# Optimization experiments

Measured on AMD Instinct MI355X. Metric: run time of the kernel, lower is better.

Reference implementation:

```python
import jax, jax.numpy as jnp
import numpy as np

IN_SHAPE = 4096
H_S = 250        # sender_hidden
H_R = 100        # receiver_hidden
MAX_LEN = 30     # message_shape[0]
VOCAB = 40       # message_shape[1]; EOS = VOCAB-1
OUT_CLS = 512 ** 2  # out_shape[1] ** out_shape[0]


def lstm_cell(x, h, c, W_ih, W_hh, b_ih, b_hh):
    # PyTorch LSTM cell: gate order i, f, g, o
    gates = W_ih @ x + b_ih + W_hh @ h + b_hh
    i, f, g, o = jnp.split(gates, 4)
    c_new = jax.nn.sigmoid(f) * c + jax.nn.sigmoid(i) * jnp.tanh(g)
    h_new = jax.nn.sigmoid(o) * jnp.tanh(c_new)
    return h_new, c_new


def setup_inputs() -> dict:
    key = jax.random.key(0)
    ks = jax.random.split(key, 16)
    s = 0.05
    return {
        "x": jax.random.normal(ks[0], (IN_SHAPE,), dtype=jnp.float32),
        "gumbel_noise": jax.random.gumbel(ks[1], (MAX_LEN, VOCAB), dtype=jnp.float32),
        "W_s1": jax.random.normal(ks[2], (H_S, IN_SHAPE)) * s,
        "b_s1": jnp.zeros((H_S,), jnp.float32),
        "W_ih1": jax.random.normal(ks[3], (4 * H_S, VOCAB)) * s,
        "W_hh1": jax.random.normal(ks[4], (4 * H_S, H_S)) * s,
        "b_ih1": jnp.zeros((4 * H_S,), jnp.float32),
        "b_hh1": jnp.zeros((4 * H_S,), jnp.float32),
        "W_p": jax.random.normal(ks[5], (VOCAB, H_S)) * s,
        "b_p": jnp.zeros((VOCAB,), jnp.float32),
        "W_ih2": jax.random.normal(ks[6], (4 * H_R, VOCAB)) * s,
        "W_hh2": jax.random.normal(ks[7], (4 * H_R, H_R)) * s,
        "b_ih2": jnp.zeros((4 * H_R,), jnp.float32),
        "b_hh2": jnp.zeros((4 * H_R,), jnp.float32),
        "W_r": jax.random.normal(ks[8], (OUT_CLS, H_R)) * s,
        "b_r": jnp.zeros((OUT_CLS,), jnp.float32),
    }


def reference(x, gumbel_noise, W_s1, b_s1, W_ih1, W_hh1, b_ih1, b_hh1,
              W_p, b_p, W_ih2, W_hh2, b_ih2, b_hh2, W_r, b_r):
    dt = x.dtype
    eos = jax.nn.one_hot(VOCAB - 1, VOCAB, dtype=dt)
    # sender: h0 = relu(sender1(x)), c0 = 0, first input = sos = zeros
    h0 = jax.nn.relu(W_s1 @ x + b_s1)
    c0 = jnp.zeros((H_S,), dt)
    sos = jnp.zeros((VOCAB,), dt)
    is_last = jnp.arange(MAX_LEN) == MAX_LEN - 1

    def sender_step(carry, inp):
        h, c, sym, done = carry
        g, last = inp
        nh, nc = lstm_cell(sym, h, c, W_ih1, W_hh1, b_ih1, b_hh1)
        logits = W_p @ nh + b_p
        soft = jax.nn.softmax(logits + g)  # gumbel_softmax, tau=1
        idx = jnp.argmax(soft)
        hard = jax.nn.one_hot(idx, VOCAB, dtype=dt)
        st = hard + soft - jax.lax.stop_gradient(soft)  # straight-through
        # at max length the original appends the plain EOS constant
        emit = jnp.where(last & ~done, eos, st)
        emit = jnp.where(done, eos, emit)
        valid = ~done  # this symbol is part of the message
        new_done = done | (idx == VOCAB - 1) | last
        h = jnp.where(done, h, nh)
        c = jnp.where(done, c, nc)
        sym = jnp.where(done, sym, emit)
        return (h, c, sym, new_done), (emit, valid)

    _, (msg, valid) = jax.lax.scan(
        sender_step, (h0, c0, sos, jnp.array(False)), (gumbel_noise, is_last))

    # receiver LSTM: consume message up to and including first EOS (freeze after)
    def recv_step(carry, inp):
        h, c = carry
        sym, v = inp
        nh, nc = lstm_cell(sym, h, c, W_ih2, W_hh2, b_ih2, b_hh2)
        return (jnp.where(v, nh, h), jnp.where(v, nc, c)), None

    (hR, _), _ = jax.lax.scan(
        recv_step, (jnp.zeros((H_R,), dt), jnp.zeros((H_R,), dt)), (msg, valid))
    return jax.nn.softmax(W_r @ hR + b_r)  # [OUT_CLS]
```

## Files before the change

kernel.cpp:

```cpp
#include <hip/hip_runtime.h>
#include <math.h>

#define HS    250
#define HRr   100
#define VOC   40
#define TMAX  30
#define NCLS  262144
#define KS    10
#define RPB   25

#define WS_FLAGS 0
#define WS_MFLAG 32
#define WS_SUMS  64
#define WS_NH    448
#define WS_LP    960
#define WS_MSG   1792
#define WS_HR    3008

#define ATOMIC_ST_REL(p, v) __hip_atomic_store((p), (v), __ATOMIC_RELEASE, __HIP_MEMORY_SCOPE_AGENT)
#define ATOMIC_ST_RLX(p, v) __hip_atomic_store((p), (v), __ATOMIC_RELAXED, __HIP_MEMORY_SCOPE_AGENT)
#define ATOMIC_LD_RLX(p)    __hip_atomic_load((p), __ATOMIC_RELAXED, __HIP_MEMORY_SCOPE_AGENT)

__device__ __forceinline__ float sigf(float x) { return 1.f / (1.f + expf(-x)); }

__device__ __forceinline__ float lanebc(float v, int l) {
  return __int_as_float(__builtin_amdgcn_readlane(__float_as_int(v), l));
}

#define SENDER_GATES(P, HV)                                   \
  {                                                           \
    _Pragma("unroll")                                         \
    for (int i = 0; i < 64; i += 4) {                         \
      a0 += whh[i    ] * lanebc(HV, i    );                   \
      a1 += whh[i + 1] * lanebc(HV, i + 1);                   \
      a2 += whh[i + 2] * lanebc(HV, i + 2);                   \
      a3 += whh[i + 3] * lanebc(HV, i + 3);                   \
    }                                                         \
    _Pragma("unroll")                                         \
    for (int i = 0; i < 10; i += 2) {                         \
      a0 += wih[i    ] * lanebc(sv, (P) * 10 + i    );        \
      a1 += wih[i + 1] * lanebc(sv, (P) * 10 + i + 1);        \
    }                                                         \
  }

#define RED(x) ((part[(x)] + part[100 + (x)]) + (part[200 + (x)] + part[300 + (x)]))

#define SPIN_FLAGS(need_)                                                     \
  {                                                                           \
    int v;                                                                    \
    do {                                                                      \
      v = (lane < KS) ? ATOMIC_LD_RLX(&flags[lane]) : (need_);                \
    } while (!__all(v >= (need_)));                                           \
  }

__global__ __launch_bounds__(512, 2) void k_sender(
    const float* __restrict__ x,
    const float* __restrict__ W_s1,  const float* __restrict__ b_s1,
    const float* __restrict__ gum,
    const float* __restrict__ W_ih1, const float* __restrict__ W_hh1,
    const float* __restrict__ b_ih1, const float* __restrict__ b_hh1,
    const float* __restrict__ W_p,   const float* __restrict__ b_p,
    const float* __restrict__ W_ih2, const float* __restrict__ W_hh2,
    const float* __restrict__ b_ih2, const float* __restrict__ b_hh2,
    float* __restrict__ ws) {
  __shared__ float part[512];
  __shared__ float symL[VOC];
  __shared__ float h0L[32];
  __shared__ int   ctrl;
  __shared__ float gL[400];
  __shared__ float hL[HRr];
  __shared__ int   rawL;

  const int b    = blockIdx.x;
  const int t0   = threadIdx.x;
  const int lane = t0 & 63;
  const int w    = t0 >> 6;

  int*   flags = (int*)ws;
  int*   mflag = (int*)ws + WS_MFLAG;
  float* nh    = ws + WS_NH;
  float* lp    = ws + WS_LP;
  float* msg   = ws + WS_MSG;

  if (b < KS) {
    const int p    = w & 3;
    const int lr   = ((w >> 2) << 6) + lane;
    const bool gact = (lr < 100);
    const int gi   = lr / 25, rr = lr % 25;
    const int grow = gi * 250 + b * RPB + rr;

    float whh[64], wih[10], bsum = 0.f;
    if (gact) {
      #pragma unroll
      for (int i = 0; i < 64; i++) {
        int k = p * 64 + i;
        whh[i] = (k < HS) ? W_hh1[(size_t)grow * HS + k] : 0.f;
      }
      #pragma unroll
      for (int i = 0; i < 10; i++) wih[i] = W_ih1[grow * VOC + p * 10 + i];
      bsum = b_ih1[grow] + b_hh1[grow];
    }
    float wps[RPB];
    float bpv = 0.f;
    if (w == 0) {
      #pragma unroll
      for (int r = 0; r < RPB; r++)
        wps[r] = (lane < VOC) ? W_p[lane * HS + b * RPB + r] : 0.f;
      bpv = (lane < VOC) ? b_p[lane] : 0.f;
    }

    {
      const int nr = (w == 7) ? 4 : 3;
      for (int j = 0; j < nr; ++j) {
        const int r = 3 * w + j;
        const float4* wr = (const float4*)(W_s1 + (size_t)(b * RPB + r) * 4096);
        const float4* xr = (const float4*)x;
        float a0 = 0.f, a1 = 0.f, a2 = 0.f, a3 = 0.f;
        #pragma unroll
        for (int q = 0; q < 16; ++q) {
          float4 w4 = wr[lane + (q << 6)], x4 = xr[lane + (q << 6)];
          a0 += w4.x * x4.x; a1 += w4.y * x4.y; a2 += w4.z * x4.z; a3 += w4.w * x4.w;
        }
        float acc = (a0 + a1) + (a2 + a3);
        #pragma unroll
        for (int o = 32; o; o >>= 1) acc += __shfl_down(acc, o);
        if (lane == 0) h0L[r] = acc + b_s1[b * RPB + r];
      }
    }
    __syncthreads();
    if (w == 0) {
      float hn0 = fmaxf(h0L[lane < RPB ? lane : 0], 0.f);
      if (lane < RPB) ATOMIC_ST_RLX(&nh[b * RPB + lane], hn0);
      if (lane == 0)  ATOMIC_ST_REL(&flags[b], 1);
      SPIN_FLAGS(1)
    }
    __syncthreads();

    float hv0, hv1, hv2, hv3;
    {
      const float* sl = nh;
      hv0 = ATOMIC_LD_RLX(&sl[lane]);
      hv1 = ATOMIC_LD_RLX(&sl[64 + lane]);
      hv2 = ATOMIC_LD_RLX(&sl[128 + lane]);
      float x3 = ATOMIC_LD_RLX(&sl[192 + lane]);
      hv3 = (192 + lane < HS) ? x3 : 0.f;
    }
    float sv = 0.f;
    float c  = 0.f;

    for (int s = 0; s < TMAX; ++s) {
      const int parity = (s + 1) & 1;
      float gv = 0.f;
      if (w == 0) gv = gum[s * VOC + (lane < VOC ? lane : 0)];

      if (gact) {
        float a0 = bsum, a1 = 0.f, a2 = 0.f, a3 = 0.f;
        if      (p == 0) SENDER_GATES(0, hv0)
        else if (p == 1) SENDER_GATES(1, hv1)
        else if (p == 2) SENDER_GATES(2, hv2)
        else             SENDER_GATES(3, hv3)
        part[p * 100 + lr] = (a0 + a1) + (a2 + a3);
      }
      __syncthreads();

      if (w == 0) {
        float gi_ = RED(lane);
        float gf_ = RED(25 + lane);
        float gg_ = RED(50 + lane);
        float go_ = RED(75 + lane);
        float ig = sigf(gi_), fg = sigf(gf_), gg = tanhf(gg_), og = sigf(go_);
        float cn = fg * c + ig * gg; c = cn;
        float hn = og * tanhf(cn);
        float lpv = 0.f;
        #pragma unroll
        for (int r = 0; r < RPB; ++r) lpv += wps[r] * lanebc(hn, r);
        float* slot = nh + parity * 256;
        float* lps  = lp + parity * 400;
        if (lane < RPB) ATOMIC_ST_RLX(&slot[b * RPB + lane], hn);
        if (lane < VOC) ATOMIC_ST_RLX(&lps[b * VOC + lane], lpv);
        if (lane == 0)  ATOMIC_ST_REL(&flags[b], s + 2);
        SPIN_FLAGS(s + 2)
      }
      __syncthreads();

      {
        const float* sl = nh + parity * 256;
        hv0 = ATOMIC_LD_RLX(&sl[lane]);
        hv1 = ATOMIC_LD_RLX(&sl[64 + lane]);
        hv2 = ATOMIC_LD_RLX(&sl[128 + lane]);
        float x3 = ATOMIC_LD_RLX(&sl[192 + lane]);
        hv3 = (192 + lane < HS) ? x3 : 0.f;
      }

      if (w == 0) {
        float lg = -INFINITY;
        if (lane < VOC) {
          float acc = bpv + gv;
          const float* ls = lp + parity * 400;
          #pragma unroll
          for (int j = 0; j < KS; ++j) acc += ATOMIC_LD_RLX(&ls[j * VOC + lane]);
          lg = acc;
        }
        float v = lg; int bi = lane;
        #pragma unroll
        for (int o = 32; o; o >>= 1) {
          float ov = __shfl_down(v, o);
          int   oi = __shfl_down(bi, o);
          if (ov > v) { v = ov; bi = oi; }
        }
        float m  = __shfl(v, 0);
        int  idx = __shfl(bi, 0);
        float e = (lane < VOC) ? expf(lg - m) : 0.f;
        float ssum = e;
        #pragma unroll
        for (int o = 32; o; o >>= 1) ssum += __shfl_down(ssum, o);
        ssum = __shfl(ssum, 0);
        float soft = e / ssum;
        float hard = (lane == idx) ? 1.f : 0.f;
        float st   = (hard + soft) - soft;
        float emit = (s == TMAX - 1) ? ((lane == VOC - 1) ? 1.f : 0.f) : st;
        if (lane < VOC) {
          symL[lane] = emit;
          if (b == 0) ATOMIC_ST_RLX(&msg[s * VOC + lane], emit);
        }
        if (lane == 0) {
          int d = (idx == VOC - 1 || s == TMAX - 1) ? 1 : 0;
          ctrl = d;
          if (b == 0) ATOMIC_ST_REL(mflag, (s + 1) | (d << 16));
        }
      }
      __syncthreads();
      sv = (lane < VOC) ? symL[lane] : 0.f;
      if (ctrl) break;
    }
  } else {
    const bool act = (t0 < 400);
    float wih2[VOC], whh2[HRr], bsum2 = 0.f;
    if (act) {
      #pragma unroll
      for (int i = 0; i < VOC; i++) wih2[i] = W_ih2[t0 * VOC + i];
      #pragma unroll
      for (int i = 0; i < HRr; i++) whh2[i] = W_hh2[t0 * HRr + i];
      bsum2 = b_ih2[t0] + b_hh2[t0];
    }
    float c2 = 0.f, rv0 = 0.f, rv1 = 0.f;

    for (int t = 0; t < TMAX; ++t) {
      if (w == 0) {
        int raw;
        do { raw = ATOMIC_LD_RLX(mflag); } while ((raw & 0xFFFF) < t + 1);
        if (lane == 0) rawL = raw;
      }
      __syncthreads();
      const int raw = rawL;
      float sv2 = (lane < VOC) ? ATOMIC_LD_RLX(&msg[t * VOC + lane]) : 0.f;
      if (act) {
        float a0 = bsum2, a1 = 0.f, a2 = 0.f, a3 = 0.f;
        #pragma unroll
        for (int i = 0; i < VOC; i += 4) {
          a0 += wih2[i    ] * lanebc(sv2, i    );
          a1 += wih2[i + 1] * lanebc(sv2, i + 1);
          a2 += wih2[i + 2] * lanebc(sv2, i + 2);
          a3 += wih2[i + 3] * lanebc(sv2, i + 3);
        }
        #pragma unroll
        for (int i = 0; i < 64; i += 4) {
          a0 += whh2[i    ] * lanebc(rv0, i    );
          a1 += whh2[i + 1] * lanebc(rv0, i + 1);
          a2 += whh2[i + 2] * lanebc(rv0, i + 2);
          a3 += whh2[i + 3] * lanebc(rv0, i + 3);
        }
        #pragma unroll
        for (int i = 0; i < 36; i += 4) {
          a0 += whh2[64 + i    ] * lanebc(rv1, i    );
          a1 += whh2[64 + i + 1] * lanebc(rv1, i + 1);
          a2 += whh2[64 + i + 2] * lanebc(rv1, i + 2);
          a3 += whh2[64 + i + 3] * lanebc(rv1, i + 3);
        }
        gL[t0] = (a0 + a1) + (a2 + a3);
      }
      __syncthreads();
      if (t0 < HRr) {
        float ig = sigf(gL[t0]);
        float fg = sigf(gL[100 + t0]);
        float gg = tanhf(gL[200 + t0]);
        float og = sigf(gL[300 + t0]);
        float cn = fg * c2 + ig * gg; c2 = cn;
        hL[t0] = og * tanhf(cn);
      }
      __syncthreads();
      rv0 = hL[lane];
      rv1 = (lane < 36) ? hL[64 + lane] : 0.f;
      if ((raw >> 16) != 0 && (raw & 0xFFFF) == t + 1) break;
    }
    if (t0 < HRr) ws[WS_HR + t0] = hL[t0];
  }
}

__global__ __launch_bounds__(256) void k_out(
    const float* __restrict__ W_r, const float* __restrict__ b_r,
    float* __restrict__ ws, float* __restrict__ out) {
  __shared__ float4 h4[25];
  __shared__ float  red[4];
  const int t0 = threadIdx.x;
  if (t0 < 25) h4[t0] = ((const float4*)(ws + WS_HR))[t0];
  __syncthreads();
  const int lane = t0 & 63;
  const int wv   = t0 >> 6;
  const int c0   = lane & 3;
  const int row  = (blockIdx.x << 6) + (wv << 4) + (lane >> 2);
  const float4* wr = (const float4*)(W_r + (size_t)row * HRr);
  float acc = 0.f;
  #pragma unroll
  for (int j = 0; j < 7; ++j) {
    int ch = 4 * j + c0;
    if (ch < 25) {
      float4 w4 = wr[ch]; float4 hq = h4[ch];
      acc += w4.x * hq.x + w4.y * hq.y + w4.z * hq.z + w4.w * hq.w;
    }
  }
  acc += __shfl_xor(acc, 1);
  acc += __shfl_xor(acc, 2);
  float e = expf(acc + b_r[row]);
  if (c0 == 0) out[row] = e;
  float es = (c0 == 0) ? e : 0.f;
  #pragma unroll
  for (int o = 32; o; o >>= 1) es += __shfl_down(es, o);
  if (lane == 0) red[wv] = es;
  __syncthreads();
  if (t0 == 0)
    atomicAdd(&ws[WS_SUMS + (blockIdx.x & 63)], (red[0] + red[1]) + (red[2] + red[3]));
}

__global__ __launch_bounds__(256) void k_scale(const float* __restrict__ ws,
                                               float* __restrict__ out) {
  float s = ws[WS_SUMS + (threadIdx.x & 63)];
  #pragma unroll
  for (int o = 1; o < 64; o <<= 1) s += __shfl_xor(s, o);
  const float rinv = 1.f / s;
  const int i = blockIdx.x * 256 + threadIdx.x;
  float4 e = ((const float4*)out)[i];
  e.x *= rinv; e.y *= rinv; e.z *= rinv; e.w *= rinv;
  ((float4*)out)[i] = e;
}

extern "C" void kernel_launch(void* const* d_in, const int* in_sizes, int n_in,
                              void* d_out, int out_size, void* d_ws, size_t ws_size,
                              hipStream_t stream) {
  const float* x     = (const float*)d_in[0];
  const float* gum   = (const float*)d_in[1];
  const float* W_s1  = (const float*)d_in[2];
  const float* b_s1  = (const float*)d_in[3];
  const float* W_ih1 = (const float*)d_in[4];
  const float* W_hh1 = (const float*)d_in[5];
  const float* b_ih1 = (const float*)d_in[6];
  const float* b_hh1 = (const float*)d_in[7];
  const float* W_p   = (const float*)d_in[8];
  const float* b_p   = (const float*)d_in[9];
  const float* W_ih2 = (const float*)d_in[10];
  const float* W_hh2 = (const float*)d_in[11];
  const float* b_ih2 = (const float*)d_in[12];
  const float* b_hh2 = (const float*)d_in[13];
  const float* W_r   = (const float*)d_in[14];
  const float* b_r   = (const float*)d_in[15];
  float* ws  = (float*)d_ws;
  float* out = (float*)d_out;

  (void)hipMemsetAsync(d_ws, 0, 768, stream);
  k_sender<<<KS + 1,   512, 0, stream>>>(x, W_s1, b_s1, gum, W_ih1, W_hh1,
                                         b_ih1, b_hh1, W_p, b_p,
                                         W_ih2, W_hh2, b_ih2, b_hh2, ws);
  k_out   <<<NCLS/64,  256, 0, stream>>>(W_r, b_r, ws, out);
  k_scale <<<NCLS/1024,256, 0, stream>>>(ws, out);
}
```

Baseline: 323.2 us.

## Replace flag-based grid sync with tagged value words and redundant per-block sampling

Each cross-block value (hidden state, logit partials, message symbols) is now stored as a 64-bit word holding a step tag and the float, so consumers spin directly on the data instead of on separate release flags. Every sender block recomputes the softmax/argmax sampling itself, which removes the extra __syncthreads and the shared control broadcast per step. The receiver polls the tagged message words directly. The output GEMV is reorganised so each block covers 128 rows, with half-wave row groups and paired float2 stores. The cost is a larger workspace memset, wider spin loads, and reliance on relaxed atomics to keep tag and value consistent.

Result: no change. 324.9 us (+0.5%).

```diff
diff --git a/kernel.cpp b/kernel.cpp
--- a/kernel.cpp
+++ b/kernel.cpp
@@ -9,23 +9,26 @@
 #define KS    10
 #define RPB   25
 
-#define WS_FLAGS 0
-#define WS_MFLAG 32
-#define WS_SUMS  64
-#define WS_NH    448
-#define WS_LP    960
-#define WS_MSG   1792
-#define WS_HR    3008
-
-#define ATOMIC_ST_REL(p, v) __hip_atomic_store((p), (v), __ATOMIC_RELEASE, __HIP_MEMORY_SCOPE_AGENT)
-#define ATOMIC_ST_RLX(p, v) __hip_atomic_store((p), (v), __ATOMIC_RELAXED, __HIP_MEMORY_SCOPE_AGENT)
-#define ATOMIC_LD_RLX(p)    __hip_atomic_load((p), __ATOMIC_RELAXED, __HIP_MEMORY_SCOPE_AGENT)
+typedef unsigned long long ull;
+
+#define PKNH(wsp, par) ((ull*)(wsp) + (size_t)(par) * 256)
+#define PKLP(wsp, par) ((ull*)(wsp) + 512 + (size_t)(par) * 400)
+#define PKMSG(wsp)     ((ull*)(wsp) + 1312)
+#define WS_SUMS 5024
+#define WS_HR   5088
+#define WS_ZERO_BYTES 20352
+
+#define AST(p, v) __hip_atomic_store((p), (v), __ATOMIC_RELAXED, __HIP_MEMORY_SCOPE_AGENT)
+#define ALD(p)    __hip_atomic_load((p), __ATOMIC_RELAXED, __HIP_MEMORY_SCOPE_AGENT)
 
 __device__ __forceinline__ float sigf(float x) { return 1.f / (1.f + expf(-x)); }
-
 __device__ __forceinline__ float lanebc(float v, int l) {
   return __int_as_float(__builtin_amdgcn_readlane(__float_as_int(v), l));
 }
+__device__ __forceinline__ ull packtv(unsigned tag, float v) {
+  return ((ull)tag << 32) | (ull)__float_as_uint(v);
+}
+__device__ __forceinline__ float lowf(ull w) { return __uint_as_float((unsigned)w); }
 
 #define SENDER_GATES(P, HV)                                   \
   {                                                           \
@@ -45,14 +48,6 @@
 
 #define RED(x) ((part[(x)] + part[100 + (x)]) + (part[200 + (x)] + part[300 + (x)]))
 
-#define SPIN_FLAGS(need_)                                                     \
-  {                                                                           \
-    int v;                                                                    \
-    do {                                                                      \
-      v = (lane < KS) ? ATOMIC_LD_RLX(&flags[lane]) : (need_);                \
-    } while (!__all(v >= (need_)));                                           \
-  }
-
 __global__ __launch_bounds__(512, 2) void k_sender(
     const float* __restrict__ x,
     const float* __restrict__ W_s1,  const float* __restrict__ b_s1,
@@ -63,24 +58,15 @@
     const float* __restrict__ W_ih2, const float* __restrict__ W_hh2,
     const float* __restrict__ b_ih2, const float* __restrict__ b_hh2,
     float* __restrict__ ws) {
-  __shared__ float part[512];
-  __shared__ float symL[VOC];
+  __shared__ float part[400];
   __shared__ float h0L[32];
-  __shared__ int   ctrl;
   __shared__ float gL[400];
   __shared__ float hL[HRr];
-  __shared__ int   rawL;
 
   const int b    = blockIdx.x;
   const int t0   = threadIdx.x;
   const int lane = t0 & 63;
   const int w    = t0 >> 6;
-
-  int*   flags = (int*)ws;
-  int*   mflag = (int*)ws + WS_MFLAG;
-  float* nh    = ws + WS_NH;
-  float* lp    = ws + WS_LP;
-  float* msg   = ws + WS_MSG;
 
   if (b < KS) {
     const int p    = w & 3;
@@ -101,13 +87,12 @@
       bsum = b_ih1[grow] + b_hh1[grow];
     }
     float wps[RPB];
-    float bpv = 0.f;
     if (w == 0) {
       #pragma unroll
       for (int r = 0; r < RPB; r++)
         wps[r] = (lane < VOC) ? W_p[lane * HS + b * RPB + r] : 0.f;
-      bpv = (lane < VOC) ? b_p[lane] : 0.f;
-    }
+    }
+    const float bpv = (lane < VOC) ? b_p[lane] : 0.f;
 
     {
       const int nr = (w == 7) ? 4 : 3;
@@ -128,30 +113,86 @@
       }
     }
     __syncthreads();
-    if (w == 0) {
-      float hn0 = fmaxf(h0L[lane < RPB ? lane : 0], 0.f);
-      if (lane < RPB) ATOMIC_ST_RLX(&nh[b * RPB + lane], hn0);
-      if (lane == 0)  ATOMIC_ST_REL(&flags[b], 1);
-      SPIN_FLAGS(1)
-    }
-    __syncthreads();
-
-    float hv0, hv1, hv2, hv3;
-    {
-      const float* sl = nh;
-      hv0 = ATOMIC_LD_RLX(&sl[lane]);
-      hv1 = ATOMIC_LD_RLX(&sl[64 + lane]);
-      hv2 = ATOMIC_LD_RLX(&sl[128 + lane]);
-      float x3 = ATOMIC_LD_RLX(&sl[192 + lane]);
-      hv3 = (192 + lane < HS) ? x3 : 0.f;
-    }
+    if (w == 0 && lane < RPB) {
+      float hn0 = fmaxf(h0L[lane], 0.f);
+      AST(&PKNH(ws, 1)[b * RPB + lane], packtv(1u, hn0));
+    }
+
+    float c  = 0.f;
     float sv = 0.f;
-    float c  = 0.f;
-
-    for (int s = 0; s < TMAX; ++s) {
-      const int parity = (s + 1) & 1;
+    const bool h3v = (192 + lane) < HS;
+
+    for (int s = 0; s <= TMAX; ++s) {
+      const unsigned need = (unsigned)(s + 1);
+      const int par = (s + 1) & 1;
       float gv = 0.f;
-      if (w == 0) gv = gum[s * VOC + (lane < VOC ? lane : 0)];
+      if (s > 0 && lane < VOC) gv = gum[(s - 1) * VOC + lane];
+
+      const ull* nhp = PKNH(ws, par);
+      const ull* lpp = PKLP(ws, par);
+      const bool lact = (s > 0) && (lane < VOC);
+      ull hw0, hw1, hw2, hw3;
+      ull lw0 = 0, lw1 = 0, lw2 = 0, lw3 = 0, lw4 = 0,
+          lw5 = 0, lw6 = 0, lw7 = 0, lw8 = 0, lw9 = 0;
+      for (;;) {
+        hw0 = ALD(&nhp[lane]);
+        hw1 = ALD(&nhp[64 + lane]);
+        hw2 = ALD(&nhp[128 + lane]);
+        hw3 = h3v ? ALD(&nhp[192 + lane]) : ((ull)need << 32);
+        bool ok = (unsigned)(hw0 >> 32) == need && (unsigned)(hw1 >> 32) == need &&
+                  (unsigned)(hw2 >> 32) == need && (unsigned)(hw3 >> 32) == need;
+        if (lact) {
+          lw0 = ALD(&lpp[0 * VOC + lane]); lw1 = ALD(&lpp[1 * VOC + lane]);
+          lw2 = ALD(&lpp[2 * VOC + lane]); lw3 = ALD(&lpp[3 * VOC + lane]);
+          lw4 = ALD(&lpp[4 * VOC + lane]); lw5 = ALD(&lpp[5 * VOC + lane]);
+          lw6 = ALD(&lpp[6 * VOC + lane]); lw7 = ALD(&lpp[7 * VOC + lane]);
+          lw8 = ALD(&lpp[8 * VOC + lane]); lw9 = ALD(&lpp[9 * VOC + lane]);
+          ok = ok && (unsigned)(lw0 >> 32) == need && (unsigned)(lw1 >> 32) == need &&
+                     (unsigned)(lw2 >> 32) == need && (unsigned)(lw3 >> 32) == need &&
+                     (unsigned)(lw4 >> 32) == need && (unsigned)(lw5 >> 32) == need &&
+                     (unsigned)(lw6 >> 32) == need && (unsigned)(lw7 >> 32) == need &&
+                     (unsigned)(lw8 >> 32) == need && (unsigned)(lw9 >> 32) == need;
+        }
+        if (__all(ok)) break;
+      }
+      float hv0 = lowf(hw0), hv1 = lowf(hw1), hv2 = lowf(hw2);
+      float hv3 = h3v ? lowf(hw3) : 0.f;
+
+      if (s > 0) {
+        float lg = -INFINITY;
+        if (lane < VOC) {
+          float acc = bpv + gv;
+          acc += lowf(lw0); acc += lowf(lw1); acc += lowf(lw2); acc += lowf(lw3);
+          acc += lowf(lw4); acc += lowf(lw5); acc += lowf(lw6); acc += lowf(lw7);
+          acc += lowf(lw8); acc += lowf(lw9);
+          lg = acc;
+        }
+        float v = lg; int bi = lane;
+        #pragma unroll
+        for (int o = 32; o; o >>= 1) {
+          float ov = __shfl_down(v, o);
+          int   oi = __shfl_down(bi, o);
+          if (ov > v) { v = ov; bi = oi; }
+        }
+        float m  = __shfl(v, 0);
+        int  idx = __shfl(bi, 0);
+        float e = (lane < VOC) ? expf(lg - m) : 0.f;
+        float ssum = e;
+        #pragma unroll
+        for (int o = 32; o; o >>= 1) ssum += __shfl_down(ssum, o);
+        ssum = __shfl(ssum, 0);
+        float soft = e / ssum;
+        float hard = (lane == idx) ? 1.f : 0.f;
+        float st   = (hard + soft) - soft;
+        const bool last = (s - 1 == TMAX - 1);
+        float emit = last ? ((lane == VOC - 1) ? 1.f : 0.f) : st;
+        const bool done = (idx == VOC - 1) || last;
+        if (b == 0 && w == 0 && lane < VOC)
+          AST(&PKMSG(ws)[(s - 1) * VOC + lane],
+              packtv((unsigned)s | (done ? 0x10000u : 0u), emit));
+        sv = (lane < VOC) ? emit : 0.f;
+        if (done) break;
+      }
 
       if (gact) {
         float a0 = bsum, a1 = 0.f, a2 = 0.f, a3 = 0.f;
@@ -164,74 +205,21 @@
       __syncthreads();
 
       if (w == 0) {
-        float gi_ = RED(lane);
-        float gf_ = RED(25 + lane);
-        float gg_ = RED(50 + lane);
-        float go_ = RED(75 + lane);
+        float gi_ = RED(lane < RPB ? lane : 0);
+        float gf_ = RED(25 + (lane < RPB ? lane : 0));
+        float gg_ = RED(50 + (lane < RPB ? lane : 0));
+        float go_ = RED(75 + (lane < RPB ? lane : 0));
         float ig = sigf(gi_), fg = sigf(gf_), gg = tanhf(gg_), og = sigf(go_);
         float cn = fg * c + ig * gg; c = cn;
         float hn = og * tanhf(cn);
-        float lpv = 0.f;
-        #pragma unroll
-        for (int r = 0; r < RPB; ++r) lpv += wps[r] * lanebc(hn, r);
-        float* slot = nh + parity * 256;
-        float* lps  = lp + parity * 400;
-        if (lane < RPB) ATOMIC_ST_RLX(&slot[b * RPB + lane], hn);
-        if (lane < VOC) ATOMIC_ST_RLX(&lps[b * VOC + lane], lpv);
-        if (lane == 0)  ATOMIC_ST_REL(&flags[b], s + 2);
-        SPIN_FLAGS(s + 2)
-      }
-      __syncthreads();
-
-      {
-        const float* sl = nh + parity * 256;
-        hv0 = ATOMIC_LD_RLX(&sl[lane]);
-        hv1 = ATOMIC_LD_RLX(&sl[64 + lane]);
-        hv2 = ATOMIC_LD_RLX(&sl[128 + lane]);
-        float x3 = ATOMIC_LD_RLX(&sl[192 + lane]);
-        hv3 = (192 + lane < HS) ? x3 : 0.f;
-      }
-
-      if (w == 0) {
-        float lg = -INFINITY;
-        if (lane < VOC) {
-          float acc = bpv + gv;
-          const float* ls = lp + parity * 400;
-          #pragma unroll
-          for (int j = 0; j < KS; ++j) acc += ATOMIC_LD_RLX(&ls[j * VOC + lane]);
-          lg = acc;
-        }
-        float v = lg; int bi = lane;
-        #pragma unroll
-        for (int o = 32; o; o >>= 1) {
-          float ov = __shfl_down(v, o);
-          int   oi = __shfl_down(bi, o);
-          if (ov > v) { v = ov; bi = oi; }
-        }
-        float m  = __shfl(v, 0);
-        int  idx = __shfl(bi, 0);
-        float e = (lane < VOC) ? expf(lg - m) : 0.f;
-        float ssum = e;
-        #pragma unroll
-        for (int o = 32; o; o >>= 1) ssum += __shfl_down(ssum, o);
-        ssum = __shfl(ssum, 0);
-        float soft = e / ssum;
-        float hard = (lane == idx) ? 1.f : 0.f;
-        float st   = (hard + soft) - soft;
-        float emit = (s == TMAX - 1) ? ((lane == VOC - 1) ? 1.f : 0.f) : st;
-        if (lane < VOC) {
-          symL[lane] = emit;
-          if (b == 0) ATOMIC_ST_RLX(&msg[s * VOC + lane], emit);
-        }
-        if (lane == 0) {
-          int d = (idx == VOC - 1 || s == TMAX - 1) ? 1 : 0;
-          ctrl = d;
-          if (b == 0) ATOMIC_ST_REL(mflag, (s + 1) | (d << 16));
-        }
-      }
-      __syncthreads();
-      sv = (lane < VOC) ? symL[lane] : 0.f;
-      if (ctrl) break;
+        float lpsum = 0.f;
+        #pragma unroll
+        for (int r = 0; r < RPB; ++r) lpsum += wps[r] * lanebc(hn, r);
+        const unsigned nt = (unsigned)(s + 2);
+        const int np = (s + 2) & 1;
+        if (lane < RPB) AST(&PKNH(ws, np)[b * RPB + lane], packtv(nt, hn));
+        if (lane < VOC) AST(&PKLP(ws, np)[b * VOC + lane], packtv(nt, lpsum));
+      }
     }
   } else {
     const bool act = (t0 < 400);
@@ -246,14 +234,16 @@
     float c2 = 0.f, rv0 = 0.f, rv1 = 0.f;
 
     for (int t = 0; t < TMAX; ++t) {
-      if (w == 0) {
-        int raw;
-        do { raw = ATOMIC_LD_RLX(mflag); } while ((raw & 0xFFFF) < t + 1);
-        if (lane == 0) rawL = raw;
-      }
-      __syncthreads();
-      const int raw = rawL;
-      float sv2 = (lane < VOC) ? ATOMIC_LD_RLX(&msg[t * VOC + lane]) : 0.f;
+      const bool mv = (lane < VOC);
+      ull mw = 0;
+      for (;;) {
+        if (mv) mw = ALD(&PKMSG(ws)[t * VOC + lane]);
+        bool ok = !mv || ((unsigned)(mw >> 32) & 0xFFFFu) == (unsigned)(t + 1);
+        if (__all(ok)) break;
+      }
+      const unsigned tag0 = (unsigned)__shfl((int)(mw >> 32), 0);
+      const bool done = (tag0 & 0x10000u) != 0;
+      float sv2 = mv ? lowf(mw) : 0.f;
       if (act) {
         float a0 = bsum2, a1 = 0.f, a2 = 0.f, a3 = 0.f;
         #pragma unroll
@@ -291,7 +281,7 @@
       __syncthreads();
       rv0 = hL[lane];
       rv1 = (lane < 36) ? hL[64 + lane] : 0.f;
-      if ((raw >> 16) != 0 && (raw & 0xFFFF) == t + 1) break;
+      if (done) break;
     }
     if (t0 < HRr) ws[WS_HR + t0] = hL[t0];
   }
@@ -307,26 +297,28 @@
   __syncthreads();
   const int lane = t0 & 63;
   const int wv   = t0 >> 6;
-  const int c0   = lane & 3;
-  const int row  = (blockIdx.x << 6) + (wv << 4) + (lane >> 2);
-  const float4* wr = (const float4*)(W_r + (size_t)row * HRr);
-  float acc = 0.f;
-  #pragma unroll
-  for (int j = 0; j < 7; ++j) {
-    int ch = 4 * j + c0;
-    if (ch < 25) {
-      float4 w4 = wr[ch]; float4 hq = h4[ch];
-      acc += w4.x * hq.x + w4.y * hq.y + w4.z * hq.z + w4.w * hq.w;
-    }
+  const int sl   = lane & 31;
+  const int hf   = lane >> 5;
+  const int base = blockIdx.x * 128 + wv * 32;
+  float accs = 0.f;
+  #pragma unroll 4
+  for (int i = 0; i < 16; ++i) {
+    const int row = base + 2 * i + hf;
+    float v = 0.f;
+    if (sl < 25) {
+      float4 w4 = ((const float4*)W_r)[(size_t)row * 25 + sl];
+      float4 hq = h4[sl];
+      v = w4.x * hq.x + w4.y * hq.y + w4.z * hq.z + w4.w * hq.w;
+    }
+    #pragma unroll
+    for (int o = 16; o; o >>= 1) v += __shfl_down(v, o, 32);
+    float e = 0.f;
+    if (sl == 0) { e = expf(v + b_r[row]); accs += e; }
+    float eB = __shfl(e, 32);
+    if (lane == 0) ((float2*)out)[(base + 2 * i) >> 1] = make_float2(e, eB);
   }
-  acc += __shfl_xor(acc, 1);
-  acc += __shfl_xor(acc, 2);
-  float e = expf(acc + b_r[row]);
-  if (c0 == 0) out[row] = e;
-  float es = (c0 == 0) ? e : 0.f;
-  #pragma unroll
-  for (int o = 32; o; o >>= 1) es += __shfl_down(es, o);
-  if (lane == 0) red[wv] = es;
+  accs += __shfl_down(accs, 32);
+  if (lane == 0) red[wv] = accs;
   __syncthreads();
   if (t0 == 0)
     atomicAdd(&ws[WS_SUMS + (blockIdx.x & 63)], (red[0] + red[1]) + (red[2] + red[3]));
@@ -366,10 +358,10 @@
   float* ws  = (float*)d_ws;
   float* out = (float*)d_out;
 
-  (void)hipMemsetAsync(d_ws, 0, 768, stream);
+  (void)hipMemsetAsync(d_ws, 0, WS_ZERO_BYTES, stream);
   k_sender<<<KS + 1,   512, 0, stream>>>(x, W_s1, b_s1, gum, W_ih1, W_hh1,
                                          b_ih1, b_hh1, W_p, b_p,
                                          W_ih2, W_hh2, b_ih2, b_hh2, ws);
-  k_out   <<<NCLS/64,  256, 0, stream>>>(W_r, b_r, ws, out);
+  k_out   <<<NCLS/128, 256, 0, stream>>>(W_r, b_r, ws, out);
   k_scale <<<NCLS/1024,256, 0, stream>>>(ws, out);
 }
```
